# Optimization experiments

Measured on AMD Instinct MI355X. Metric: run time of the kernel, lower is better.

The kernel has to match this reference:

```python
import jax, jax.numpy as jnp
import numpy as np

T_VID = 129  # TACoS iou grid size

def make_iou_mask_map():
    m = np.zeros((129, 129), np.float32)
    for i in range(0, 128):
        m[i, 1 + i:min(i + 17, 129)] = 1.0
    for i in range(0, 128 - 16, 2):
        m[i, list(range(18 + i, min(33 + i, 129), 2))] = 1.0
    for i in range(0, 128 - 32, 4):
        m[i, list(range(36 + i, min(65 + i, 129), 4))] = 1.0
    for i in range(0, 128 - 64, 8):
        m[i, list(range(72 + i, 129, 8))] = 1.0
    return jnp.asarray(m)

def setup_inputs() -> dict:
    key = jax.random.key(0)
    B, L, T, D, CH, V = 8, 100, T_VID, 512, 512, 1000
    ks = jax.random.split(key, 20)
    g = lambda k, shp, fan: jax.random.normal(k, shp, jnp.float32) * (1.0 / np.sqrt(fan))
    return {
        'hidden_states_text': jax.random.normal(ks[0], (B, L, D), jnp.float32),
        'hidden_states_object': jax.random.normal(ks[1], (B, T, D), jnp.float32),
        # final_mlp (text head): D->CH->V
        'w_t1': g(ks[2], (D, CH), D), 'b_t1': jnp.zeros((CH,), jnp.float32),
        'w_t2': g(ks[3], (CH, V), CH), 'b_t2': jnp.zeros((V,), jnp.float32),
        # final_mlp_2: D -> 3D (+ReLU)
        'w2': g(ks[4], (D, 3 * D), D), 'b2': jnp.zeros((3 * D,), jnp.float32),
        # final_mlp_3: 3D -> CH -> 3
        'w3a': g(ks[5], (3 * D, CH), 3 * D), 'b3a': jnp.zeros((CH,), jnp.float32),
        'w3b': g(ks[6], (CH, 3), CH), 'b3b': jnp.zeros((3,), jnp.float32),
        # final_mlp_s/e/c: D -> CH -> 1
        'w_s1': g(ks[7], (D, CH), D), 'b_s1': jnp.zeros((CH,), jnp.float32),
        'w_s2': g(ks[8], (CH, 1), CH), 'b_s2': jnp.zeros((1,), jnp.float32),
        'w_e1': g(ks[9], (D, CH), D), 'b_e1': jnp.zeros((CH,), jnp.float32),
        'w_e2': g(ks[10], (CH, 1), CH), 'b_e2': jnp.zeros((1,), jnp.float32),
        'w_c1': g(ks[11], (D, CH), D), 'b_c1': jnp.zeros((CH,), jnp.float32),
        'w_c2': g(ks[12], (CH, 1), CH), 'b_c2': jnp.zeros((1,), jnp.float32),
    }

def _head(x, w1, b1, w2, b2):
    return jax.nn.relu(x @ w1 + b1) @ w2 + b2

def reference(hidden_states_text, hidden_states_object,
              w_t1, b_t1, w_t2, b_t2, w2, b2, w3a, b3a, w3b, b3b,
              w_s1, b_s1, w_s2, b_s2, w_e1, b_e1, w_e2, b_e2,
              w_c1, b_c1, w_c2, b_c2):
    D = hidden_states_object.shape[-1]
    T = hidden_states_object.shape[1]
    # text head (dropout is identity at inference)
    logits_text = _head(hidden_states_text, w_t1, b_t1, w_t2, b_t2)
    # final_mlp_2 then split into start/center/end streams, each [B,T,D]
    h = jax.nn.relu(hidden_states_object @ w2 + b2)
    hs, hc, he = h[..., :D], h[..., D:2 * D], h[..., 2 * D:]
    # final_mlp_3 first linear decomposed over the concat blocks:
    # grid[b,i,j] = W_s.hs[i] + W_c.hc[(i+j)//2] + W_e.he[j] + b  (same math as
    # cat(repeat(hs), gather(hc), repeat(he)) @ w3a, without the 3D grid)
    ps = hc @ w3a[D:2 * D]            # [B,T,CH] (center projection, gathered below)
    pS = hs @ w3a[:D]                 # [B,T,CH]
    pE = he @ w3a[2 * D:]             # [B,T,CH]
    idx = (jnp.arange(T)[:, None] + jnp.arange(T)[None, :]) // 2  # [T,T] center index
    grid = pS[:, :, None, :] + ps[:, idx, :] + pE[:, None, :, :] + b3a  # [B,T,T,CH]
    logits_iou = (jax.nn.relu(grid) @ w3b + b3b)  # [B,T,T,3]
    logits_iou = jnp.transpose(logits_iou, (0, 3, 1, 2))  # [B,3,T,T]
    logits_visual = jnp.concatenate([
        _head(hs, w_s1, b_s1, w_s2, b_s2),
        _head(he, w_e1, b_e1, w_e2, b_e2),
        _head(hc, w_c1, b_c1, w_c2, b_c2)], axis=-1)  # [B,T,3]
    return logits_text, logits_visual, logits_iou, make_iou_mask_map()
```

## Files before the change

kernel.cpp:

```cpp
#include <hip/hip_runtime.h>
#include <hip/hip_bf16.h>

typedef unsigned short ushort_t;
typedef __attribute__((ext_vector_type(4))) unsigned short u16x4;
typedef __attribute__((ext_vector_type(8))) short bf16x8;
typedef __attribute__((ext_vector_type(4))) float f32x4;

constexpr int BB = 8, LL = 100, TT = 129, DD = 512, CH = 512, VV = 1000;
constexpr int M_TXT = BB * LL;
constexpr int M_OBJ = BB * TT;
constexpr int P_SLAB = M_OBJ * DD;
constexpr int N_IOU = BB * 3 * TT * TT;
constexpr int N_VIS = 3 * M_OBJ;
constexpr int N_MASK = TT * TT;

constexpr int OUT_TEXT = 0;
constexpr int OUT_VIS  = M_TXT * VV;
constexpr int OUT_IOU  = OUT_VIS + N_VIS;
constexpr int OUT_MASK = OUT_IOU + N_IOU;

constexpr size_t WB_TEXT = 0;
constexpr size_t WB_OBJ  = WB_TEXT + 819200;
constexpr size_t WB_WT1  = WB_OBJ  + 1056768;
constexpr size_t WB_WT2  = WB_WT1  + 524288;
constexpr size_t WB_W2T  = WB_WT2  + 1024000;
constexpr size_t WB_W3AT = WB_W2T  + 1572864;
constexpr size_t WB_WS1T = WB_W3AT + 1572864;
constexpr size_t WB_WE1T = WB_WS1T + 524288;
constexpr size_t WB_WC1T = WB_WE1T + 524288;
constexpr size_t WB_T1   = WB_WC1T + 524288;
constexpr size_t WB_H    = WB_T1   + 819200;
constexpr size_t WB_P    = WB_H    + 3170304;

__device__ __forceinline__ ushort_t f2bf(float x) {
    __hip_bfloat16 h = __float2bfloat16(x);
    return *(ushort_t*)&h;
}

struct TDesc { const float* src; ushort_t* dst; int R, C, tiles, ctiles; };
struct PrepArgs {
    const float* act_a; ushort_t* act_da; int na4;
    const float* act_b; ushort_t* act_db; int nb4;
    int nact_blocks, nwt_blocks;
    TDesc t[7];
    const float *b3b, *bs2, *be2, *bc2;
    float* out;
};

__global__ __launch_bounds__(256)
void prep_kernel(PrepArgs pa)
{
    const int bxg = blockIdx.x;
    if (bxg < pa.nact_blocks) {
        int gid = bxg * 256 + threadIdx.x;
        const float* src; ushort_t* dst;
        if (gid < pa.na4) { src = pa.act_a + gid * 4; dst = pa.act_da + gid * 4; }
        else { gid -= pa.na4; if (gid >= pa.nb4) return; src = pa.act_b + gid * 4; dst = pa.act_db + gid * 4; }
        f32x4 v = *(const f32x4*)src;
        dst[0] = f2bf(v[0]); dst[1] = f2bf(v[1]); dst[2] = f2bf(v[2]); dst[3] = f2bf(v[3]);
        return;
    }
    if (bxg < pa.nact_blocks + pa.nwt_blocks) {
        __shared__ float tl[32][33];
        int bx = bxg - pa.nact_blocks;
        TDesc e;
        #pragma unroll
        for (int i = 0; i < 7; ++i) {
            if (bx < pa.t[i].tiles) { e = pa.t[i]; break; }
            bx -= pa.t[i].tiles;
        }
        const int t = threadIdx.x;
        const int tx = t & 31, ty = t >> 5;
        const int rt = bx / e.ctiles, ct = bx - rt * e.ctiles;
        #pragma unroll
        for (int i = 0; i < 4; ++i) {
            const int r = rt * 32 + ty + i * 8, c = ct * 32 + tx;
            tl[ty + i * 8][tx] = (r < e.R && c < e.C) ? e.src[(size_t)r * e.C + c] : 0.0f;
        }
        __syncthreads();
        const int drl = t >> 3, dcl = (t & 7) << 2;
        const int grow = ct * 32 + drl;
        if (grow < e.C) {
            u16x4 v;
            #pragma unroll
            for (int u = 0; u < 4; ++u) v[u] = f2bf(tl[dcl + u][drl]);
            *(u16x4*)&e.dst[(size_t)grow * e.R + rt * 32 + dcl] = v;
        }
        return;
    }
    int g = (bxg - pa.nact_blocks - pa.nwt_blocks) * 256 + threadIdx.x;
    if (g < N_IOU) {
        const int bk = g / (TT * TT);
        const int k = bk - (bk / 3) * 3;
        pa.out[OUT_IOU + g] = pa.b3b[k];
        return;
    }
    g -= N_IOU;
    if (g < N_VIS) {
        const int head = g - (g / 3) * 3;
        const float bias = head == 0 ? pa.bs2[0] : (head == 1 ? pa.be2[0] : pa.bc2[0]);
        pa.out[OUT_VIS + g] = bias;
        return;
    }
    g -= N_VIS;
    if (g < N_MASK) {
        const int i = g / TT, j = g - i * TT;
        const int d = j - i;
        bool v = false;
        if (i < 128 && d >= 1 && d <= 16) v = true;
        if (!v && (i & 1) == 0 && i <= 110 && d >= 18 && d <= 32 && (d & 1) == 0) v = true;
        if (!v && (i & 3) == 0 && i <= 92  && d >= 36 && d <= 64 && (d & 3) == 0) v = true;
        if (!v && (i & 7) == 0 && i <= 56  && d >= 72 && (d & 7) == 0) v = true;
        pa.out[OUT_MASK + g] = v ? 1.0f : 0.0f;
    }
}

struct GemmDesc {
    const ushort_t* A; int lda;
    const ushort_t* Bt; int ldb;
    const float* bias;
    void* C; int ldc;
    int M, N, K;
    int mode;
    const float* w2head;
    float* vbase;
    int vhead;
    int ntiles, ntx;
};
struct GemmArgs { GemmDesc d[7]; };

__global__ __launch_bounds__(256)
void gemm_mfma(GemmArgs args)
{
    int bx = blockIdx.x, zi = 0;
    while (bx >= args.d[zi].ntiles) { bx -= args.d[zi].ntiles; ++zi; }
    const GemmDesc g = args.d[zi];
    const int tyT = bx / g.ntx, txT = bx - tyT * g.ntx;
    const int m0 = tyT * 128, n0 = txT * 128;

    __shared__ ushort_t ldsA[2][2][128 * 32];
    __shared__ ushort_t ldsB[2][2][128 * 32];

    const int tid = threadIdx.x;
    const int w = tid >> 6, l = tid & 63;
    const int wr = w >> 1, wc = w & 1;

    const int srow = l >> 2;
    const int scol = (l & 3) << 3;
    const int wbase = w << 4;

    f32x4 acc[4][4];
    #pragma unroll
    for (int mi = 0; mi < 4; ++mi)
        #pragma unroll
        for (int ni = 0; ni < 4; ++ni)
            acc[mi][ni] = f32x4{0.f, 0.f, 0.f, 0.f};

    const int nk = g.K >> 6;

    auto stage = [&](int buf, int k0) {
        #pragma unroll
        for (int ks = 0; ks < 2; ++ks) {
            #pragma unroll
            for (int q = 0; q < 2; ++q) {
                int gm = m0 + (q << 6) + wbase + srow; if (gm >= g.M) gm = g.M - 1;
                __builtin_amdgcn_global_load_lds(
                    (const __attribute__((address_space(1))) unsigned int*)(g.A + (size_t)gm * g.lda + k0 + (ks << 5) + scol),
                    (__attribute__((address_space(3))) unsigned int*)&ldsA[buf][ks][((q << 6) + wbase) * 32],
                    16, 0, 0);
                int gn = n0 + (q << 6) + wbase + srow; if (gn >= g.N) gn = g.N - 1;
                __builtin_amdgcn_global_load_lds(
                    (const __attribute__((address_space(1))) unsigned int*)(g.Bt + (size_t)gn * g.ldb + k0 + (ks << 5) + scol),
                    (__attribute__((address_space(3))) unsigned int*)&ldsB[buf][ks][((q << 6) + wbase) * 32],
                    16, 0, 0);
            }
        }
    };

    stage(0, 0);
    int cur = 0;
    const int fr = l & 15, kq = (l >> 4) << 3;

    for (int kt = 0; kt < nk; ++kt) {
        __syncthreads();
        if (kt + 1 < nk) stage(cur ^ 1, (kt + 1) << 6);
        #pragma unroll
        for (int ks = 0; ks < 2; ++ks) {
            bf16x8 av[4], bv[4];
            #pragma unroll
            for (int mi = 0; mi < 4; ++mi)
                av[mi] = *(const bf16x8*)&ldsA[cur][ks][((wr << 6) + (mi << 4) + fr) * 32 + kq];
            #pragma unroll
            for (int ni = 0; ni < 4; ++ni)
                bv[ni] = *(const bf16x8*)&ldsB[cur][ks][((wc << 6) + (ni << 4) + fr) * 32 + kq];
            #pragma unroll
            for (int mi = 0; mi < 4; ++mi)
                #pragma unroll
                for (int ni = 0; ni < 4; ++ni)
                    acc[mi][ni] = __builtin_amdgcn_mfma_f32_16x16x32_bf16(av[mi], bv[ni], acc[mi][ni], 0, 0, 0);
        }
        cur ^= 1;
    }

    const int rq = (l >> 4) << 2;
    if (g.mode == 2) {
        float s[4][4];
        #pragma unroll
        for (int mi = 0; mi < 4; ++mi)
            #pragma unroll
            for (int r = 0; r < 4; ++r) s[mi][r] = 0.f;
        #pragma unroll
        for (int ni = 0; ni < 4; ++ni) {
            const int col = n0 + (wc << 6) + (ni << 4) + fr;
            const float bb = g.bias[col];
            const float wv = g.w2head[col];
            #pragma unroll
            for (int mi = 0; mi < 4; ++mi)
                #pragma unroll
                for (int r = 0; r < 4; ++r) {
                    float v = fmaxf(acc[mi][ni][r] + bb, 0.f);
                    s[mi][r] = fmaf(v, wv, s[mi][r]);
                }
        }
        #pragma unroll
        for (int off = 1; off < 16; off <<= 1)
            #pragma unroll
            for (int mi = 0; mi < 4; ++mi)
                #pragma unroll
                for (int r = 0; r < 4; ++r)
                    s[mi][r] += __shfl_xor(s[mi][r], off);
        if (fr == 0) {
            #pragma unroll
            for (int mi = 0; mi < 4; ++mi)
                #pragma unroll
                for (int r = 0; r < 4; ++r) {
                    const int row = m0 + (wr << 6) + (mi << 4) + rq + r;
                    if (row < g.M) atomicAdd(&g.vbase[row * 3 + g.vhead], s[mi][r]);
                }
        }
    } else {
        #pragma unroll
        for (int ni = 0; ni < 4; ++ni) {
            const int col = n0 + (wc << 6) + (ni << 4) + fr;
            const float bb = (g.bias && col < g.N) ? g.bias[col] : 0.f;
            #pragma unroll
            for (int mi = 0; mi < 4; ++mi)
                #pragma unroll
                for (int r = 0; r < 4; ++r) {
                    const int row = m0 + (wr << 6) + (mi << 4) + rq + r;
                    if (row < g.M && col < g.N) {
                        float v = acc[mi][ni][r] + bb;
                        if (g.mode == 1) {
                            v = fmaxf(v, 0.f);
                            ((ushort_t*)g.C)[(size_t)row * g.ldc + col] = f2bf(v);
                        } else {
                            ((float*)g.C)[(size_t)row * g.ldc + col] = v;
                        }
                    }
                }
        }
    }
}

__global__ __launch_bounds__(256)
void iou_kernel(const float* __restrict__ P, const float* __restrict__ w3b,
                float* __restrict__ out)
{
    __shared__ __align__(16) float sP[96 * 132];
    __shared__ __align__(16) float sW[384];

    const int tid = threadIdx.x;
    const int b = blockIdx.z >> 1;
    const int half = blockIdx.z & 1;
    const int i0 = blockIdx.y * 32, j0 = blockIdx.x * 32;
    const int idx0 = (i0 + j0) >> 1;
    const int par = (i0 + j0) & 1;

    const int ii = tid >> 4, jj = tid & 15;
    const int o = ((ii + jj + par) >> 1) + 32;

    const f32x4 z4 = {0.f, 0.f, 0.f, 0.f};
    f32x4 av00[3], av01[3], av10[3], av11[3];
    #pragma unroll
    for (int k = 0; k < 3; ++k) { av00[k] = z4; av01[k] = z4; av10[k] = z4; av11[k] = z4; }

    for (int ph = 0; ph < 2; ++ph) {
        const int c0 = (half << 8) + (ph << 7);
        if (ph) __syncthreads();
        for (int f = tid; f < 384; f += 256) {
            const int k = f >> 7, c = f & 127;
            sW[f] = w3b[(c0 + c) * 3 + k];
        }
        for (int f = tid; f < 3072; f += 256) {
            const int row = f >> 5;
            const int pos = (f & 31) << 2;
            const int a = row >> 5;
            const int r = row & 31;
            int rg = (a == 0) ? (i0 + r) : (a == 1) ? (idx0 + r) : (j0 + r);
            if (rg > 128) rg = 128;
            f32x4 v = *(const f32x4*)&P[(size_t)a * P_SLAB + ((size_t)(b * TT) + rg) * DD + c0 + pos];
            *(f32x4*)&sP[row * 132 + pos] = v;
        }
        __syncthreads();

        const float* rs0 = &sP[ii * 132];
        const float* rs1 = &sP[(ii + 16) * 132];
        const float* rp0 = &sP[o * 132];
        const float* rp1 = &sP[(o + 8) * 132];
        const float* rp2 = &sP[(o + 16) * 132];
        const float* re0 = &sP[(64 + jj) * 132];
        const float* re1 = &sP[(64 + jj + 16) * 132];

        #pragma unroll 2
        for (int c = 0; c < 128; c += 4) {
            const f32x4 s0 = *(const f32x4*)&rs0[c];
            const f32x4 s1 = *(const f32x4*)&rs1[c];
            const f32x4 p0 = *(const f32x4*)&rp0[c];
            const f32x4 p1 = *(const f32x4*)&rp1[c];
            const f32x4 p2 = *(const f32x4*)&rp2[c];
            const f32x4 e0 = *(const f32x4*)&re0[c];
            const f32x4 e1 = *(const f32x4*)&re1[c];
            const f32x4 w0 = *(const f32x4*)&sW[c];
            const f32x4 w1 = *(const f32x4*)&sW[128 + c];
            const f32x4 w2 = *(const f32x4*)&sW[256 + c];

            const f32x4 t00 = s0 + e0, t01 = s0 + e1, t10 = s1 + e0, t11 = s1 + e1;
            const f32x4 v00 = __builtin_elementwise_max(t00 + p0, z4);
            const f32x4 v01 = __builtin_elementwise_max(t01 + p1, z4);
            const f32x4 v10 = __builtin_elementwise_max(t10 + p1, z4);
            const f32x4 v11 = __builtin_elementwise_max(t11 + p2, z4);

            av00[0] = __builtin_elementwise_fma(v00, w0, av00[0]);
            av00[1] = __builtin_elementwise_fma(v00, w1, av00[1]);
            av00[2] = __builtin_elementwise_fma(v00, w2, av00[2]);
            av01[0] = __builtin_elementwise_fma(v01, w0, av01[0]);
            av01[1] = __builtin_elementwise_fma(v01, w1, av01[1]);
            av01[2] = __builtin_elementwise_fma(v01, w2, av01[2]);
            av10[0] = __builtin_elementwise_fma(v10, w0, av10[0]);
            av10[1] = __builtin_elementwise_fma(v10, w1, av10[1]);
            av10[2] = __builtin_elementwise_fma(v10, w2, av10[2]);
            av11[0] = __builtin_elementwise_fma(v11, w0, av11[0]);
            av11[1] = __builtin_elementwise_fma(v11, w1, av11[1]);
            av11[2] = __builtin_elementwise_fma(v11, w2, av11[2]);
        }
    }

    auto emit = [&](const f32x4* acc, int i, int j) {
        if (i <= 128 && j <= 128) {
            #pragma unroll
            for (int k = 0; k < 3; ++k) {
                const float s = acc[k][0] + acc[k][1] + acc[k][2] + acc[k][3];
                atomicAdd(&out[OUT_IOU + ((size_t)(b * 3 + k) * TT + i) * TT + j], s);
            }
        }
    };
    emit(av00, i0 + ii, j0 + jj);
    emit(av01, i0 + ii, j0 + jj + 16);
    emit(av10, i0 + ii + 16, j0 + jj);
    emit(av11, i0 + ii + 16, j0 + jj + 16);
}

extern "C" void kernel_launch(void* const* d_in, const int* in_sizes, int n_in,
                              void* d_out, int out_size, void* d_ws, size_t ws_size,
                              hipStream_t stream)
{
    const float* text = (const float*)d_in[0];
    const float* obj  = (const float*)d_in[1];
    const float* w_t1 = (const float*)d_in[2];
    const float* b_t1 = (const float*)d_in[3];
    const float* w_t2 = (const float*)d_in[4];
    const float* b_t2 = (const float*)d_in[5];
    const float* w2   = (const float*)d_in[6];
    const float* b2   = (const float*)d_in[7];
    const float* w3a  = (const float*)d_in[8];
    const float* b3a  = (const float*)d_in[9];
    const float* w3b  = (const float*)d_in[10];
    const float* b3b  = (const float*)d_in[11];
    const float* w_s1 = (const float*)d_in[12];
    const float* b_s1 = (const float*)d_in[13];
    const float* w_s2 = (const float*)d_in[14];
    const float* b_s2 = (const float*)d_in[15];
    const float* w_e1 = (const float*)d_in[16];
    const float* b_e1 = (const float*)d_in[17];
    const float* w_e2 = (const float*)d_in[18];
    const float* b_e2 = (const float*)d_in[19];
    const float* w_c1 = (const float*)d_in[20];
    const float* b_c1 = (const float*)d_in[21];
    const float* w_c2 = (const float*)d_in[22];
    const float* b_c2 = (const float*)d_in[23];

    float* out = (float*)d_out;
    char* ws = (char*)d_ws;
    ushort_t* text_bf = (ushort_t*)(ws + WB_TEXT);
    ushort_t* obj_bf  = (ushort_t*)(ws + WB_OBJ);
    ushort_t* wt1     = (ushort_t*)(ws + WB_WT1);
    ushort_t* wt2     = (ushort_t*)(ws + WB_WT2);
    ushort_t* w2t     = (ushort_t*)(ws + WB_W2T);
    ushort_t* w3at    = (ushort_t*)(ws + WB_W3AT);
    ushort_t* ws1t    = (ushort_t*)(ws + WB_WS1T);
    ushort_t* we1t    = (ushort_t*)(ws + WB_WE1T);
    ushort_t* wc1t    = (ushort_t*)(ws + WB_WC1T);
    ushort_t* T1      = (ushort_t*)(ws + WB_T1);
    ushort_t* H       = (ushort_t*)(ws + WB_H);
    float*    P       = (float*)(ws + WB_P);

    {
        PrepArgs pa;
        pa.act_a = text; pa.act_da = text_bf; pa.na4 = (M_TXT * DD) / 4;
        pa.act_b = obj;  pa.act_db = obj_bf;  pa.nb4 = (M_OBJ * DD) / 4;
        pa.nact_blocks = (pa.na4 + pa.nb4 + 255) / 256;
        pa.nwt_blocks = 3072;
        pa.t[0] = {w_t1, wt1, 512, 512, 256, 16};
        pa.t[1] = {w_t2, wt2, 512, 1000, 512, 32};
        pa.t[2] = {w2, w2t, 512, 1536, 768, 48};
        pa.t[3] = {w3a, w3at, 1536, 512, 768, 16};
        pa.t[4] = {w_s1, ws1t, 512, 512, 256, 16};
        pa.t[5] = {w_e1, we1t, 512, 512, 256, 16};
        pa.t[6] = {w_c1, wc1t, 512, 512, 256, 16};
        pa.b3b = b3b; pa.bs2 = b_s2; pa.be2 = b_e2; pa.bc2 = b_c2;
        pa.out = out;
        const int ninit = (N_IOU + N_VIS + N_MASK + 255) / 256;
        prep_kernel<<<dim3(pa.nact_blocks + pa.nwt_blocks + ninit), dim3(256), 0, stream>>>(pa);
    }
    {
        GemmArgs a{};
        a.d[0] = {text_bf, DD, wt1, DD, b_t1, T1, CH, M_TXT, CH, DD, 1, nullptr, nullptr, 0, 28, 4};
        a.d[1] = {obj_bf, DD, w2t, DD, b2, H, 3 * DD, M_OBJ, 3 * DD, DD, 1, nullptr, nullptr, 0, 108, 12};
        gemm_mfma<<<dim3(136), dim3(256), 0, stream>>>(a);
    }
    {
        GemmArgs a{};
        a.d[0] = {T1, CH, wt2, CH, b_t2, out + OUT_TEXT, VV, M_TXT, VV, CH, 0, nullptr, nullptr, 0, 56, 8};
        a.d[1] = {H + 0 * DD, 3 * DD, w3at + 0 * DD, 3 * DD, b3a, P + 0 * P_SLAB, DD, M_OBJ, DD, DD, 0, nullptr, nullptr, 0, 36, 4};
        a.d[2] = {H + 1 * DD, 3 * DD, w3at + 1 * DD, 3 * DD, nullptr, P + 1 * P_SLAB, DD, M_OBJ, DD, DD, 0, nullptr, nullptr, 0, 36, 4};
        a.d[3] = {H + 2 * DD, 3 * DD, w3at + 2 * DD, 3 * DD, nullptr, P + 2 * P_SLAB, DD, M_OBJ, DD, DD, 0, nullptr, nullptr, 0, 36, 4};
        a.d[4] = {H + 0 * DD, 3 * DD, ws1t, DD, b_s1, nullptr, 0, M_OBJ, CH, DD, 2, w_s2, out + OUT_VIS, 0, 36, 4};
        a.d[5] = {H + 2 * DD, 3 * DD, we1t, DD, b_e1, nullptr, 0, M_OBJ, CH, DD, 2, w_e2, out + OUT_VIS, 1, 36, 4};
        a.d[6] = {H + 1 * DD, 3 * DD, wc1t, DD, b_c1, nullptr, 0, M_OBJ, CH, DD, 2, w_c2, out + OUT_VIS, 2, 36, 4};
        gemm_mfma<<<dim3(272), dim3(256), 0, stream>>>(a);
    }
    iou_kernel<<<dim3(5, 5, 16), dim3(256), 0, stream>>>(P, w3b, out);
}
```

Measured before the change: 81.86 us.

## Move output init into first GEMM launch and widen weight transpose tiles

The bias and mask output initialisation moves out of the prep kernel and runs as extra blocks of the first GEMM launch, using dynamic shared memory. Each of those blocks now handles 1024 elements. The weight transpose now uses 32x64 tiles with 8-wide bf16 stores, which halves the transpose block count. The aim is a shorter prep kernel and wider stores. The init blocks are cheap and fill idle CUs next to the 136 GEMM tiles.

```diff
diff --git a/kernel.cpp b/kernel.cpp
--- a/kernel.cpp
+++ b/kernel.cpp
@@ -2,7 +2,7 @@
 #include <hip/hip_bf16.h>
 
 typedef unsigned short ushort_t;
-typedef __attribute__((ext_vector_type(4))) unsigned short u16x4;
+typedef __attribute__((ext_vector_type(8))) unsigned short u16x8;
 typedef __attribute__((ext_vector_type(8))) short bf16x8;
 typedef __attribute__((ext_vector_type(4))) float f32x4;
 
@@ -41,10 +41,8 @@
 struct PrepArgs {
     const float* act_a; ushort_t* act_da; int na4;
     const float* act_b; ushort_t* act_db; int nb4;
-    int nact_blocks, nwt_blocks;
+    int nact_blocks;
     TDesc t[7];
-    const float *b3b, *bs2, *be2, *bc2;
-    float* out;
 };
 
 __global__ __launch_bounds__(256)
@@ -60,58 +58,36 @@
         dst[0] = f2bf(v[0]); dst[1] = f2bf(v[1]); dst[2] = f2bf(v[2]); dst[3] = f2bf(v[3]);
         return;
     }
-    if (bxg < pa.nact_blocks + pa.nwt_blocks) {
-        __shared__ float tl[32][33];
-        int bx = bxg - pa.nact_blocks;
-        TDesc e;
-        #pragma unroll
-        for (int i = 0; i < 7; ++i) {
-            if (bx < pa.t[i].tiles) { e = pa.t[i]; break; }
-            bx -= pa.t[i].tiles;
-        }
-        const int t = threadIdx.x;
-        const int tx = t & 31, ty = t >> 5;
-        const int rt = bx / e.ctiles, ct = bx - rt * e.ctiles;
-        #pragma unroll
-        for (int i = 0; i < 4; ++i) {
-            const int r = rt * 32 + ty + i * 8, c = ct * 32 + tx;
-            tl[ty + i * 8][tx] = (r < e.R && c < e.C) ? e.src[(size_t)r * e.C + c] : 0.0f;
-        }
-        __syncthreads();
-        const int drl = t >> 3, dcl = (t & 7) << 2;
-        const int grow = ct * 32 + drl;
-        if (grow < e.C) {
-            u16x4 v;
-            #pragma unroll
-            for (int u = 0; u < 4; ++u) v[u] = f2bf(tl[dcl + u][drl]);
-            *(u16x4*)&e.dst[(size_t)grow * e.R + rt * 32 + dcl] = v;
-        }
-        return;
-    }
-    int g = (bxg - pa.nact_blocks - pa.nwt_blocks) * 256 + threadIdx.x;
-    if (g < N_IOU) {
-        const int bk = g / (TT * TT);
-        const int k = bk - (bk / 3) * 3;
-        pa.out[OUT_IOU + g] = pa.b3b[k];
-        return;
-    }
-    g -= N_IOU;
-    if (g < N_VIS) {
-        const int head = g - (g / 3) * 3;
-        const float bias = head == 0 ? pa.bs2[0] : (head == 1 ? pa.be2[0] : pa.bc2[0]);
-        pa.out[OUT_VIS + g] = bias;
-        return;
-    }
-    g -= N_VIS;
-    if (g < N_MASK) {
-        const int i = g / TT, j = g - i * TT;
-        const int d = j - i;
-        bool v = false;
-        if (i < 128 && d >= 1 && d <= 16) v = true;
-        if (!v && (i & 1) == 0 && i <= 110 && d >= 18 && d <= 32 && (d & 1) == 0) v = true;
-        if (!v && (i & 3) == 0 && i <= 92  && d >= 36 && d <= 64 && (d & 3) == 0) v = true;
-        if (!v && (i & 7) == 0 && i <= 56  && d >= 72 && (d & 7) == 0) v = true;
-        pa.out[OUT_MASK + g] = v ? 1.0f : 0.0f;
+    __shared__ float tl[32][65];
+    int bx = bxg - pa.nact_blocks;
+    TDesc e;
+    #pragma unroll
+    for (int i = 0; i < 7; ++i) {
+        if (bx < e.tiles || true) { e = pa.t[i]; if (bx < e.tiles) break; bx -= e.tiles; }
+    }
+    const int t = threadIdx.x;
+    const int rt = bx / e.ctiles, ct = bx - rt * e.ctiles;
+    {
+        const int c = t & 63, ty = t >> 6;
+        const int gc = ct * 64 + c;
+        const bool cok = gc < e.C;
+        const float* sp = e.src + (size_t)(rt * 32) * e.C + gc;
+        #pragma unroll
+        for (int i = 0; i < 8; ++i) {
+            const int rr = ty + i * 4;
+            tl[rr][c] = cok ? sp[(size_t)rr * e.C] : 0.0f;
+        }
+    }
+    __syncthreads();
+    {
+        const int dr = t >> 2, dc0 = (t & 3) << 3;
+        const int gdr = ct * 64 + dr;
+        if (gdr < e.C) {
+            u16x8 v;
+            #pragma unroll
+            for (int u = 0; u < 8; ++u) v[u] = f2bf(tl[dc0 + u][dr]);
+            *(u16x8*)&e.dst[(size_t)gdr * e.R + rt * 32 + dc0] = v;
+        }
     }
 }
 
@@ -127,19 +103,58 @@
     int vhead;
     int ntiles, ntx;
 };
-struct GemmArgs { GemmDesc d[7]; };
+struct MegaArgs {
+    GemmDesc d[7];
+    int gemm_blocks;
+    const float *b3b, *bs2, *be2, *bc2;
+    float* out;
+};
 
 __global__ __launch_bounds__(256)
-void gemm_mfma(GemmArgs args)
+void mega_kernel(MegaArgs args)
 {
+    extern __shared__ char smem[];
+    if ((int)blockIdx.x >= args.gemm_blocks) {
+        int g = (blockIdx.x - args.gemm_blocks) * 1024 + threadIdx.x * 4;
+        #pragma unroll
+        for (int u = 0; u < 4; ++u, ++g) {
+            int gg = g;
+            if (gg < N_IOU) {
+                const int bk = gg / (TT * TT);
+                const int k = bk - (bk / 3) * 3;
+                args.out[OUT_IOU + gg] = args.b3b[k];
+                continue;
+            }
+            gg -= N_IOU;
+            if (gg < N_VIS) {
+                const int head = gg - (gg / 3) * 3;
+                const float bias = head == 0 ? args.bs2[0] : (head == 1 ? args.be2[0] : args.bc2[0]);
+                args.out[OUT_VIS + gg] = bias;
+                continue;
+            }
+            gg -= N_VIS;
+            if (gg < N_MASK) {
+                const int i = gg / TT, j = gg - i * TT;
+                const int d = j - i;
+                bool v = false;
+                if (i < 128 && d >= 1 && d <= 16) v = true;
+                if (!v && (i & 1) == 0 && i <= 110 && d >= 18 && d <= 32 && (d & 1) == 0) v = true;
+                if (!v && (i & 3) == 0 && i <= 92  && d >= 36 && d <= 64 && (d & 3) == 0) v = true;
+                if (!v && (i & 7) == 0 && i <= 56  && d >= 72 && (d & 7) == 0) v = true;
+                args.out[OUT_MASK + gg] = v ? 1.0f : 0.0f;
+            }
+        }
+        return;
+    }
+
     int bx = blockIdx.x, zi = 0;
     while (bx >= args.d[zi].ntiles) { bx -= args.d[zi].ntiles; ++zi; }
     const GemmDesc g = args.d[zi];
     const int tyT = bx / g.ntx, txT = bx - tyT * g.ntx;
     const int m0 = tyT * 128, n0 = txT * 128;
 
-    __shared__ ushort_t ldsA[2][2][128 * 32];
-    __shared__ ushort_t ldsB[2][2][128 * 32];
+    ushort_t* ldsA = (ushort_t*)smem;
+    ushort_t* ldsB = (ushort_t*)smem + 16384;
 
     const int tid = threadIdx.x;
     const int w = tid >> 6, l = tid & 63;
@@ -161,17 +176,18 @@
     auto stage = [&](int buf, int k0) {
         #pragma unroll
         for (int ks = 0; ks < 2; ++ks) {
+            const int sb = ((buf * 2 + ks) << 12);
             #pragma unroll
             for (int q = 0; q < 2; ++q) {
                 int gm = m0 + (q << 6) + wbase + srow; if (gm >= g.M) gm = g.M - 1;
                 __builtin_amdgcn_global_load_lds(
                     (const __attribute__((address_space(1))) unsigned int*)(g.A + (size_t)gm * g.lda + k0 + (ks << 5) + scol),
-                    (__attribute__((address_space(3))) unsigned int*)&ldsA[buf][ks][((q << 6) + wbase) * 32],
+                    (__attribute__((address_space(3))) unsigned int*)(ldsA + sb + (((q << 6) + wbase) << 5)),
                     16, 0, 0);
                 int gn = n0 + (q << 6) + wbase + srow; if (gn >= g.N) gn = g.N - 1;
                 __builtin_amdgcn_global_load_lds(
                     (const __attribute__((address_space(1))) unsigned int*)(g.Bt + (size_t)gn * g.ldb + k0 + (ks << 5) + scol),
-                    (__attribute__((address_space(3))) unsigned int*)&ldsB[buf][ks][((q << 6) + wbase) * 32],
+                    (__attribute__((address_space(3))) unsigned int*)(ldsB + sb + (((q << 6) + wbase) << 5)),
                     16, 0, 0);
             }
         }
@@ -186,13 +202,14 @@
         if (kt + 1 < nk) stage(cur ^ 1, (kt + 1) << 6);
         #pragma unroll
         for (int ks = 0; ks < 2; ++ks) {
+            const int sb = ((cur * 2 + ks) << 12);
             bf16x8 av[4], bv[4];
             #pragma unroll
             for (int mi = 0; mi < 4; ++mi)
-                av[mi] = *(const bf16x8*)&ldsA[cur][ks][((wr << 6) + (mi << 4) + fr) * 32 + kq];
+                av[mi] = *(const bf16x8*)(ldsA + sb + ((((wr << 6) + (mi << 4) + fr) << 5) + kq));
             #pragma unroll
             for (int ni = 0; ni < 4; ++ni)
-                bv[ni] = *(const bf16x8*)&ldsB[cur][ks][((wc << 6) + (ni << 4) + fr) * 32 + kq];
+                bv[ni] = *(const bf16x8*)(ldsB + sb + ((((wc << 6) + (ni << 4) + fr) << 5) + kq));
             #pragma unroll
             for (int mi = 0; mi < 4; ++mi)
                 #pragma unroll
@@ -409,27 +426,26 @@
         pa.act_a = text; pa.act_da = text_bf; pa.na4 = (M_TXT * DD) / 4;
         pa.act_b = obj;  pa.act_db = obj_bf;  pa.nb4 = (M_OBJ * DD) / 4;
         pa.nact_blocks = (pa.na4 + pa.nb4 + 255) / 256;
-        pa.nwt_blocks = 3072;
-        pa.t[0] = {w_t1, wt1, 512, 512, 256, 16};
-        pa.t[1] = {w_t2, wt2, 512, 1000, 512, 32};
-        pa.t[2] = {w2, w2t, 512, 1536, 768, 48};
-        pa.t[3] = {w3a, w3at, 1536, 512, 768, 16};
-        pa.t[4] = {w_s1, ws1t, 512, 512, 256, 16};
-        pa.t[5] = {w_e1, we1t, 512, 512, 256, 16};
-        pa.t[6] = {w_c1, wc1t, 512, 512, 256, 16};
-        pa.b3b = b3b; pa.bs2 = b_s2; pa.be2 = b_e2; pa.bc2 = b_c2;
-        pa.out = out;
-        const int ninit = (N_IOU + N_VIS + N_MASK + 255) / 256;
-        prep_kernel<<<dim3(pa.nact_blocks + pa.nwt_blocks + ninit), dim3(256), 0, stream>>>(pa);
+        pa.t[0] = {w_t1, wt1, 512, 512, 128, 8};
+        pa.t[1] = {w_t2, wt2, 512, 1000, 256, 16};
+        pa.t[2] = {w2, w2t, 512, 1536, 384, 24};
+        pa.t[3] = {w3a, w3at, 1536, 512, 384, 8};
+        pa.t[4] = {w_s1, ws1t, 512, 512, 128, 8};
+        pa.t[5] = {w_e1, we1t, 512, 512, 128, 8};
+        pa.t[6] = {w_c1, wc1t, 512, 512, 128, 8};
+        prep_kernel<<<dim3(pa.nact_blocks + 1536), dim3(256), 0, stream>>>(pa);
     }
     {
-        GemmArgs a{};
+        MegaArgs a{};
         a.d[0] = {text_bf, DD, wt1, DD, b_t1, T1, CH, M_TXT, CH, DD, 1, nullptr, nullptr, 0, 28, 4};
         a.d[1] = {obj_bf, DD, w2t, DD, b2, H, 3 * DD, M_OBJ, 3 * DD, DD, 1, nullptr, nullptr, 0, 108, 12};
-        gemm_mfma<<<dim3(136), dim3(256), 0, stream>>>(a);
+        a.gemm_blocks = 136;
+        a.b3b = b3b; a.bs2 = b_s2; a.be2 = b_e2; a.bc2 = b_c2; a.out = out;
+        const int ninit = (N_IOU + N_VIS + N_MASK + 1023) / 1024;
+        mega_kernel<<<dim3(136 + ninit), dim3(256), 65536, stream>>>(a);
     }
     {
-        GemmArgs a{};
+        MegaArgs a{};
         a.d[0] = {T1, CH, wt2, CH, b_t2, out + OUT_TEXT, VV, M_TXT, VV, CH, 0, nullptr, nullptr, 0, 56, 8};
         a.d[1] = {H + 0 * DD, 3 * DD, w3at + 0 * DD, 3 * DD, b3a, P + 0 * P_SLAB, DD, M_OBJ, DD, DD, 0, nullptr, nullptr, 0, 36, 4};
         a.d[2] = {H + 1 * DD, 3 * DD, w3at + 1 * DD, 3 * DD, nullptr, P + 1 * P_SLAB, DD, M_OBJ, DD, DD, 0, nullptr, nullptr, 0, 36, 4};
@@ -437,7 +453,9 @@
         a.d[4] = {H + 0 * DD, 3 * DD, ws1t, DD, b_s1, nullptr, 0, M_OBJ, CH, DD, 2, w_s2, out + OUT_VIS, 0, 36, 4};
         a.d[5] = {H + 2 * DD, 3 * DD, we1t, DD, b_e1, nullptr, 0, M_OBJ, CH, DD, 2, w_e2, out + OUT_VIS, 1, 36, 4};
         a.d[6] = {H + 1 * DD, 3 * DD, wc1t, DD, b_c1, nullptr, 0, M_OBJ, CH, DD, 2, w_c2, out + OUT_VIS, 2, 36, 4};
-        gemm_mfma<<<dim3(272), dim3(256), 0, stream>>>(a);
+        a.gemm_blocks = 272;
+        a.b3b = b3b; a.bs2 = b_s2; a.be2 = b_e2; a.bc2 = b_c2; a.out = out;
+        mega_kernel<<<dim3(272), dim3(256), 65536, stream>>>(a);
     }
     iou_kernel<<<dim3(5, 5, 16), dim3(256), 0, stream>>>(P, w3b, out);
 }
```

Result: faster. 77.35 us (-5.5%).
